# Performance work log

Hardware: AMD Instinct MI355X
Metric: run time of the kernel (lower is better)

Reference implementation:

```python
import jax, jax.numpy as jnp
import numpy as np

N = 100000
E = 1600000
H = 128
IN = 16
OUT = 16
L = 3
G = 256  # number of graphs
EPS = 1e-12


def setup_inputs() -> dict:
    key = jax.random.key(0)
    ks = jax.random.split(key, 24)
    s = 0.05
    inp = {
        "x": jax.random.normal(ks[0], (N, IN), jnp.float32),
        "pos": jax.random.normal(ks[1], (N, 3), jnp.float32),
        "edge_index": jax.random.randint(ks[2], (2, E), 0, N, jnp.int64),
        "batch": jnp.sort(jax.random.randint(ks[3], (N,), 0, G, jnp.int64)),
        # node_lin: Linear(IN,H), ReLU, Linear(H,H)
        "node_W1": jax.random.normal(ks[4], (IN, H), jnp.float32) * s,
        "node_b1": jnp.zeros((H,), jnp.float32),
        "node_W2": jax.random.normal(ks[5], (H, H), jnp.float32) * s,
        "node_b2": jnp.zeros((H,), jnp.float32),
        # per-layer local_nn: Linear(H+4,H), ReLU, Linear(H,H)  (stacked over L)
        "local_W1": jax.random.normal(ks[6], (L, H + 4, H), jnp.float32) * s,
        "local_b1": jnp.zeros((L, H), jnp.float32),
        "local_W2": jax.random.normal(ks[7], (L, H, H), jnp.float32) * s,
        "local_b2": jnp.zeros((L, H), jnp.float32),
        # per-layer global_nn: Linear(H,H), ReLU, Linear(H,H)
        "global_W1": jax.random.normal(ks[8], (L, H, H), jnp.float32) * s,
        "global_b1": jnp.zeros((L, H), jnp.float32),
        "global_W2": jax.random.normal(ks[9], (L, H, H), jnp.float32) * s,
        "global_b2": jnp.zeros((L, H), jnp.float32),
        # heads
        "lin1_W": jax.random.normal(ks[10], (H, H // 2), jnp.float32) * s,
        "lin1_b": jnp.zeros((H // 2,), jnp.float32),
        "lin2_W": jax.random.normal(ks[11], (H // 2, OUT), jnp.float32) * s,
        "lin2_b": jnp.zeros((OUT,), jnp.float32),
    }
    return inp


def _angle(v1, v2):
    c = jnp.cross(v1, v2, axis=1)
    return jnp.arctan2(jnp.linalg.norm(c, axis=1), jnp.sum(v1 * v2, axis=1))


def reference(x, pos, edge_index, batch,
              node_W1, node_b1, node_W2, node_b2,
              local_W1, local_b1, local_W2, local_b2,
              global_W1, global_b1, global_W2, global_b2,
              lin1_W, lin1_b, lin2_W, lin2_b):
    src = edge_index[0]  # j (source)
    dst = edge_index[1]  # i (target, aggregation index)

    normal = pos / (jnp.linalg.norm(pos, axis=-1, keepdims=True) + EPS)

    pos_i, pos_j = pos[dst], pos[src]
    n_i, n_j = normal[dst], normal[src]
    pseudo = pos_j - pos_i  # [E, 3]
    # point-pair features [E, 4] (constant across layers since pos is fixed)
    ppf = jnp.stack([
        jnp.linalg.norm(pseudo, axis=1),
        _angle(n_i, pseudo),
        _angle(n_j, pseudo),
        _angle(n_i, n_j),
    ], axis=1)

    # node_lin (x is 2D -> MLP path; embedding path unused)
    h = jax.nn.relu(x @ node_W1 + node_b1) @ node_W2 + node_b2  # [N, H]

    for l in range(L):
        msg = jnp.concatenate([h[src], ppf], axis=1)  # [E, H+4]
        msg = jax.nn.relu(msg @ local_W1[l] + local_b1[l]) @ local_W2[l] + local_b2[l]
        agg = jax.ops.segment_sum(msg, dst, num_segments=N)  # scatter-add to nodes
        h = jax.nn.relu(agg @ global_W1[l] + global_b1[l]) @ global_W2[l] + global_b2[l]
        h = jax.nn.relu(h)

    out = jax.nn.relu(h @ lin1_W + lin1_b) @ lin2_W + lin2_b  # [N, OUT]
    return jax.ops.segment_sum(out, batch, num_segments=G)  # [G, OUT]
```

## Files before the change

### kernel.cpp

```cpp
#include <hip/hip_runtime.h>

#define NN 100000
#define NE 1600000
#define HD 128
#define NL 3
#define NG 256
#define NB 196
#define BCAP 56

typedef __attribute__((ext_vector_type(8))) short short8;
typedef __attribute__((ext_vector_type(4))) float floatx4;
typedef __attribute__((ext_vector_type(2))) _Float16 half2v;

static __device__ __forceinline__ unsigned short f2bf(float f) {
    unsigned int u = __float_as_uint(f);
    u += 0x7fffu + ((u >> 16) & 1u);
    return (unsigned short)(u >> 16);
}
static __device__ __forceinline__ float bf2f(unsigned short h) {
    return __uint_as_float(((unsigned int)h) << 16);
}
static __device__ __forceinline__ float angle3(float ax, float ay, float az,
                                               float bx, float by, float bz) {
    float cx = ay*bz - az*by;
    float cy = az*bx - ax*bz;
    float cz = ax*by - ay*bx;
    float cn = sqrtf(cx*cx + cy*cy + cz*cz);
    float d  = ax*bx + ay*by + az*bz;
    return atan2f(cn, d);
}

union U32H2 { unsigned int u; half2v h; };
static __device__ __forceinline__ half2v u2h(unsigned int x) { U32H2 t; t.u = x; return t.h; }
static __device__ __forceinline__ unsigned int h2u(half2v x) { U32H2 t; t.h = x; return t.u; }


struct PrepSrcs { const float* p[14]; };

__global__ void k_prep(PrepSrcs s, unsigned short* __restrict__ dst) {
    int mat = blockIdx.y;
    int N = (mat == 13) ? 64 : 128;
    int e = blockIdx.x * 256 + threadIdx.x;
    if (e >= N * 128) return;
    int n = e >> 7, k = e & 127;
    dst[mat * 16384 + n * 128 + k] = f2bf(s.p[mat][k * N + n]);
}


__global__ void k_pn(const float* __restrict__ pos, float4* __restrict__ pn, int n) {
    int i = blockIdx.x * blockDim.x + threadIdx.x;
    if (i >= n) return;
    float x = pos[3*i], y = pos[3*i+1], z = pos[3*i+2];
    float inv = 1.0f / (sqrtf(x*x + y*y + z*z) + 1e-12f);
    pn[2*i]   = make_float4(x, y, z, 0.0f);
    pn[2*i+1] = make_float4(x*inv, y*inv, z*inv, 0.0f);
}


__global__ __launch_bounds__(256) void k_bcount(const int* __restrict__ ei,
                                                int* __restrict__ bcnt, int e) {
    __shared__ int cnt[NB];
    int tid = threadIdx.x;
    for (int i = tid; i < NB; i += 256) cnt[i] = 0;
    __syncthreads();
    int i0 = blockIdx.x * 4096 + tid * 16;
    if (i0 < e) {
#pragma unroll
        for (int q = 0; q < 4; q++) {
            int4 d4 = *(const int4*)(ei + NE + i0 + q * 4);
            atomicAdd(&cnt[d4.x >> 9], 1);
            atomicAdd(&cnt[d4.y >> 9], 1);
            atomicAdd(&cnt[d4.z >> 9], 1);
            atomicAdd(&cnt[d4.w >> 9], 1);
        }
    }
    __syncthreads();
    for (int i = tid; i < NB; i += 256)
        if (cnt[i]) atomicAdd(&bcnt[i], cnt[i]);
}

__global__ void k_bscan(const int* __restrict__ bcnt, int* __restrict__ bbase,
                        int* __restrict__ bcursor, int* __restrict__ starts) {
    if (threadIdx.x == 0 && blockIdx.x == 0) {
        int acc = 0;
        for (int b = 0; b < NB; b++) {
            bbase[b] = acc; bcursor[b] = acc;
            acc += bcnt[b];
        }
        bbase[NB] = acc;
        starts[NN] = NE;
    }
}

__global__ __launch_bounds__(256) void k_bscatter(const int* __restrict__ ei,
                                                  int* __restrict__ bcursor,
                                                  unsigned int* __restrict__ bids, int e) {
    __shared__ int lcnt[NB];
    __shared__ unsigned int lbuf[NB * BCAP];
    int tid = threadIdx.x;
    for (int i = tid; i < NB; i += 256) lcnt[i] = 0;
    __syncthreads();
    int i0 = blockIdx.x * 4096 + tid * 16;
    if (i0 < e) {
#pragma unroll
        for (int q = 0; q < 4; q++) {
            int4 s4 = *(const int4*)(ei + i0 + q * 4);
            int4 d4 = *(const int4*)(ei + NE + i0 + q * 4);
            int ds[4] = {d4.x, d4.y, d4.z, d4.w};
            int ss[4] = {s4.x, s4.y, s4.z, s4.w};
#pragma unroll
            for (int r = 0; r < 4; r++) {
                int d = ds[r];
                int b = d >> 9;
                unsigned int w = ((unsigned int)(d & 511) << 17) | (unsigned int)ss[r];
                int pos = atomicAdd(&lcnt[b], 1);
                if (pos < BCAP) lbuf[b * BCAP + pos] = w;
                else { int p = atomicAdd(&bcursor[b], 1); bids[p] = w; }
            }
        }
    }
    __syncthreads();
    if (tid < NB) {
        int c = lcnt[tid];
        if (c > BCAP) c = BCAP;
        if (c > 0) {
            int base = atomicAdd(&bcursor[tid], c);
            for (int k = 0; k < c; k++) bids[base + k] = lbuf[tid * BCAP + k];
        }
    }
}

__global__ __launch_bounds__(256) void k_bfinal(const unsigned int* __restrict__ bids,
                                                const int* __restrict__ bbase,
                                                int* __restrict__ ssrc,
                                                int* __restrict__ sdst,
                                                int* __restrict__ starts,
                                                int* __restrict__ deg) {
    __shared__ int s1[512];
    __shared__ int s2[256];
    int tid = threadIdx.x;
    int b = blockIdx.x;
    int node0 = b << 9;
    int base0 = bbase[b];
    int cnt = bbase[b + 1] - base0;
    s1[2 * tid] = 0; s1[2 * tid + 1] = 0;
    __syncthreads();
    for (int j = tid; j < cnt; j += 256)
        atomicAdd(&s1[bids[base0 + j] >> 17], 1);
    __syncthreads();
    int a0 = s1[2 * tid], a1 = s1[2 * tid + 1];
    s2[tid] = a0 + a1;
    __syncthreads();
    for (int off = 1; off < 256; off <<= 1) {
        int v = (tid >= off) ? s2[tid - off] : 0;
        __syncthreads();
        s2[tid] += v;
        __syncthreads();
    }
    int pairBase = (tid ? s2[tid - 1] : 0);
    int e0 = base0 + pairBase;
    int e1 = e0 + a0;
    int n0 = node0 + 2 * tid;
    if (n0 < NN)     { starts[n0] = e0;     deg[n0] = a0; }
    if (n0 + 1 < NN) { starts[n0 + 1] = e1; deg[n0 + 1] = a1; }
    s1[2 * tid] = e0; s1[2 * tid + 1] = e1;
    __syncthreads();
    for (int j = tid; j < cnt; j += 256) {
        unsigned int w = bids[base0 + j];
        int loc = w >> 17;
        int src = (int)(w & 0x1ffffu);
        int p = atomicAdd(&s1[loc], 1);
        ssrc[p] = src;
        sdst[p] = node0 + loc;
    }
}

__global__ void k_ppf_sorted(const int* __restrict__ ssrc, const int* __restrict__ sdst,
                             const float4* __restrict__ pn,
                             uint2* __restrict__ sppf, int e) {
    int j = blockIdx.x * blockDim.x + threadIdx.x;
    if (j >= e) return;
    int s = ssrc[j];
    int d = sdst[j];
    float4 ps_ = pn[2*s], ns_ = pn[2*s+1];
    float4 pd_ = pn[2*d], nd_ = pn[2*d+1];
    float px = ps_.x - pd_.x;
    float py = ps_.y - pd_.y;
    float pz = ps_.z - pd_.z;
    float f0 = sqrtf(px*px + py*py + pz*pz);
    float f1 = angle3(nd_.x, nd_.y, nd_.z, px, py, pz);
    float f2 = angle3(ns_.x, ns_.y, ns_.z, px, py, pz);
    float f3 = angle3(nd_.x, nd_.y, nd_.z, ns_.x, ns_.y, ns_.z);
    half2v h01 = { (_Float16)f0, (_Float16)f1 };
    half2v h23 = { (_Float16)f2, (_Float16)f3 };
    uint2 w;
    w.x = h2u(h01);
    w.y = h2u(h23);
    sppf[j] = w;
}


__global__ void k_node_lin1(const float* __restrict__ x, const float* __restrict__ W1,
                            const float* __restrict__ b1, unsigned short* __restrict__ u, int n) {
    __shared__ float sW[16 * HD];
    __shared__ float sb[HD];
    __shared__ float sx[16 * 16];
    int tid = threadIdx.x;
    for (int idx = tid; idx < 16 * HD; idx += 256) sW[idx] = W1[idx];
    if (tid < HD) sb[tid] = b1[tid];
    int r0 = blockIdx.x * 16;
    for (int idx = tid; idx < 16 * 16; idx += 256) {
        int r = r0 + (idx >> 4);
        sx[idx] = (r < n) ? x[r * 16 + (idx & 15)] : 0.0f;
    }
    __syncthreads();
    int col = tid & 127;
    int rsub = tid >> 7;
    float wcol[16];
#pragma unroll
    for (int k = 0; k < 16; k++) wcol[k] = sW[k * HD + col];
    float bb = sb[col];
    for (int rr = rsub; rr < 16; rr += 2) {
        int r = r0 + rr;
        if (r >= n) break;
        float acc = bb;
#pragma unroll
        for (int k = 0; k < 16; k++) acc = fmaf(sx[rr * 16 + k], wcol[k], acc);
        u[r * HD + col] = f2bf(fmaxf(acc, 0.0f));
    }
}


#define SKT 136

struct ChainArgs {
    const unsigned short* W[4];
    const float* bias[4];
    int epi[4];
};

template <int NS, int NCL>
__global__ __launch_bounds__(256, 4) void k_chain(
    const unsigned short* __restrict__ in, ChainArgs ca,
    const int* __restrict__ deg, unsigned short* __restrict__ out, int n) {
    __shared__ unsigned short LB[128 * SKT];
    __shared__ float sbias[NS][128];
    int tid = threadIdx.x;
    int wave = tid >> 6, lane = tid & 63, quad = lane >> 4, m = lane & 15;
    int rowBase = wave * 32;
    int gBase = blockIdx.x * 128;
    floatx4 z = {0.0f, 0.0f, 0.0f, 0.0f};
    short8 a[2][4];
#pragma unroll
    for (int rt = 0; rt < 2; rt++) {
        int r = gBase + rowBase + rt * 16 + m;
        int rc = r < n ? r : n - 1;
        const unsigned short* ap = in + (size_t)rc * 128 + quad * 8;
#pragma unroll
        for (int s = 0; s < 4; s++) a[rt][s] = *(const short8*)(ap + s * 32);
    }
    if (tid < 128) {
#pragma unroll
        for (int s = 0; s < NS; s++)
            if (ca.epi[s]) sbias[s][tid] = ca.bias[s][tid];
    }
    float dvd[2][4];
#pragma unroll
    for (int rt = 0; rt < 2; rt++)
#pragma unroll
        for (int r = 0; r < 4; r++) {
            int gr = gBase + rowBase + rt * 16 + quad * 4 + r;
            dvd[rt][r] = (float)deg[gr < n ? gr : n - 1];
        }

#pragma unroll
    for (int st = 0; st < NS; st++) {
        const int NC = (st == NS - 1) ? NCL : 128;
        if (st > 0) {
#pragma unroll
            for (int rt = 0; rt < 2; rt++) {
                const unsigned short* tp = &LB[(rowBase + rt * 16 + m) * SKT + quad * 8];
#pragma unroll
                for (int s = 0; s < 4; s++) a[rt][s] = *(const short8*)(tp + s * 32);
            }
            __syncthreads();
        }
        for (int idx = tid; idx < NC * 16; idx += 256) {
            int c = idx >> 4, k8 = idx & 15;
            *(short8*)&LB[c * SKT + k8 * 8] = ((const short8*)ca.W[st])[idx];
        }
        __syncthreads();

        floatx4 acc[2][8];
#pragma unroll
        for (int rt = 0; rt < 2; rt++)
#pragma unroll
            for (int ct = 0; ct < 8; ct++) acc[rt][ct] = z;
#pragma unroll
        for (int ct = 0; ct < NC / 16; ct++) {
            const unsigned short* bp = &LB[(ct * 16 + m) * SKT + quad * 8];
#pragma unroll
            for (int s = 0; s < 4; s++) {
                short8 b = *(const short8*)(bp + s * 32);
                acc[0][ct] = __builtin_amdgcn_mfma_f32_16x16x32_bf16(a[0][s], b, acc[0][ct], 0, 0, 0);
                acc[1][ct] = __builtin_amdgcn_mfma_f32_16x16x32_bf16(a[1][s], b, acc[1][ct], 0, 0, 0);
            }
        }
        __syncthreads();

        int epi = ca.epi[st];
#pragma unroll
        for (int ct = 0; ct < NC / 16; ct++) {
            int col = ct * 16 + m;
            float bv = epi ? sbias[st][col] : 0.0f;
#pragma unroll
            for (int rt = 0; rt < 2; rt++) {
#pragma unroll
                for (int r = 0; r < 4; r++) {
                    float v = acc[rt][ct][r];
                    if (epi == 1) v += bv;
                    else if (epi == 2) v += dvd[rt][r] * bv;
                    else if (epi == 3) v = fmaxf(v + bv, 0.0f);
                    unsigned short bw = f2bf(v);
                    int row = rowBase + rt * 16 + quad * 4 + r;
                    if (st == NS - 1) {
                        int gr = gBase + row;
                        if (gr < n) out[(size_t)gr * NCL + col] = bw;
                    } else {
                        LB[row * SKT + col] = bw;
                    }
                }
            }
        }
        if (st < NS - 1) __syncthreads();
    }
}


#if __has_builtin(__builtin_amdgcn_fdot2)
#define HAVE_FDOT2 1
#else
#define HAVE_FDOT2 0
#endif

static __device__ __forceinline__ void agg_edge(unsigned int u, uint2 q,
                                                half2v wA0, half2v wB0, half2v wA1, half2v wB1,
                                                float2 bb, float& a0, float& a1) {
    float tlo = __uint_as_float(u << 16);
    float thi = __uint_as_float(u & 0xffff0000u);
#if HAVE_FDOT2
    half2v p01 = u2h(q.x), p23 = u2h(q.y);
    float g0 = __builtin_amdgcn_fdot2(p01, wA0,
               __builtin_amdgcn_fdot2(p23, wB0, bb.x + tlo, false), false);
    float g1 = __builtin_amdgcn_fdot2(p01, wA1,
               __builtin_amdgcn_fdot2(p23, wB1, bb.y + thi, false), false);
#else
    half2v p01 = u2h(q.x), p23 = u2h(q.y);
    float px = (float)p01.x, py = (float)p01.y, pz = (float)p23.x, pw = (float)p23.y;
    float g0 = fmaf(px, (float)wA0.x, fmaf(py, (float)wA0.y,
               fmaf(pz, (float)wB0.x, fmaf(pw, (float)wB0.y, bb.x + tlo))));
    float g1 = fmaf(px, (float)wA1.x, fmaf(py, (float)wA1.y,
               fmaf(pz, (float)wB1.x, fmaf(pw, (float)wB1.y, bb.y + thi))));
#endif
    a0 += fmaxf(g0, 0.0f);
    a1 += fmaxf(g1, 0.0f);
}

__global__ __launch_bounds__(256, 8) void k_agg(
    const int* __restrict__ starts, const int* __restrict__ ssrc,
    const uint2* __restrict__ sppf, const unsigned int* __restrict__ t,
    const float* __restrict__ W1p, const float* __restrict__ b1,
    unsigned int* __restrict__ S, int n) {
    int node = (blockIdx.x * 256 + threadIdx.x) >> 6;
    if (node >= n) return;
    int lane = threadIdx.x & 63;
    int c2 = lane * 2;
    float2 w0 = *(const float2*)(W1p + c2);
    float2 w1 = *(const float2*)(W1p + 128 + c2);
    float2 w2 = *(const float2*)(W1p + 256 + c2);
    float2 w3 = *(const float2*)(W1p + 384 + c2);
    float2 bb = *(const float2*)(b1 + c2);
    half2v wA0 = { (_Float16)w0.x, (_Float16)w1.x };
    half2v wB0 = { (_Float16)w2.x, (_Float16)w3.x };
    half2v wA1 = { (_Float16)w0.y, (_Float16)w1.y };
    half2v wB1 = { (_Float16)w2.y, (_Float16)w3.y };
    int e0 = __builtin_amdgcn_readfirstlane(starts[node]);
    int e1 = __builtin_amdgcn_readfirstlane(starts[node + 1]);
    float a0 = 0.0f, a1 = 0.0f;
    int e = e0;
    for (; e + 8 <= e1; e += 8) {
        int s0 = ssrc[e],     s1 = ssrc[e + 1], s2 = ssrc[e + 2], s3 = ssrc[e + 3];
        int s4 = ssrc[e + 4], s5 = ssrc[e + 5], s6 = ssrc[e + 6], s7 = ssrc[e + 7];
        uint2 q0 = sppf[e],     q1 = sppf[e + 1], q2 = sppf[e + 2], q3 = sppf[e + 3];
        uint2 q4 = sppf[e + 4], q5 = sppf[e + 5], q6 = sppf[e + 6], q7 = sppf[e + 7];
        unsigned int u0 = t[((unsigned)s0 << 6) | lane];
        unsigned int u1 = t[((unsigned)s1 << 6) | lane];
        unsigned int u2 = t[((unsigned)s2 << 6) | lane];
        unsigned int u3 = t[((unsigned)s3 << 6) | lane];
        unsigned int u4 = t[((unsigned)s4 << 6) | lane];
        unsigned int u5 = t[((unsigned)s5 << 6) | lane];
        unsigned int u6 = t[((unsigned)s6 << 6) | lane];
        unsigned int u7 = t[((unsigned)s7 << 6) | lane];
        agg_edge(u0, q0, wA0, wB0, wA1, wB1, bb, a0, a1);
        agg_edge(u1, q1, wA0, wB0, wA1, wB1, bb, a0, a1);
        agg_edge(u2, q2, wA0, wB0, wA1, wB1, bb, a0, a1);
        agg_edge(u3, q3, wA0, wB0, wA1, wB1, bb, a0, a1);
        agg_edge(u4, q4, wA0, wB0, wA1, wB1, bb, a0, a1);
        agg_edge(u5, q5, wA0, wB0, wA1, wB1, bb, a0, a1);
        agg_edge(u6, q6, wA0, wB0, wA1, wB1, bb, a0, a1);
        agg_edge(u7, q7, wA0, wB0, wA1, wB1, bb, a0, a1);
    }
    for (; e + 4 <= e1; e += 4) {
        int s0 = ssrc[e], s1 = ssrc[e + 1], s2 = ssrc[e + 2], s3 = ssrc[e + 3];
        uint2 q0 = sppf[e], q1 = sppf[e + 1], q2 = sppf[e + 2], q3 = sppf[e + 3];
        unsigned int u0 = t[((unsigned)s0 << 6) | lane];
        unsigned int u1 = t[((unsigned)s1 << 6) | lane];
        unsigned int u2 = t[((unsigned)s2 << 6) | lane];
        unsigned int u3 = t[((unsigned)s3 << 6) | lane];
        agg_edge(u0, q0, wA0, wB0, wA1, wB1, bb, a0, a1);
        agg_edge(u1, q1, wA0, wB0, wA1, wB1, bb, a0, a1);
        agg_edge(u2, q2, wA0, wB0, wA1, wB1, bb, a0, a1);
        agg_edge(u3, q3, wA0, wB0, wA1, wB1, bb, a0, a1);
    }
    for (; e < e1; e++) {
        int s0 = ssrc[e];
        uint2 q0 = sppf[e];
        unsigned int u0 = t[((unsigned)s0 << 6) | lane];
        agg_edge(u0, q0, wA0, wB0, wA1, wB1, bb, a0, a1);
    }
    unsigned int r = ((unsigned int)f2bf(a1) << 16) | f2bf(a0);
    S[(size_t)node * 64 + lane] = r;
}


__global__ void k_head2(const unsigned short* __restrict__ v, const float* __restrict__ W,
                        const float* __restrict__ b, const int* __restrict__ batch,
                        float* __restrict__ outg, int n) {
    __shared__ float sW[64 * 16];
    __shared__ float sb[16];
    __shared__ float sacc[64][17];
    __shared__ int sbid[64];
    int tid = threadIdx.x;
    for (int idx = tid; idx < 64 * 16; idx += 256) sW[idx] = W[idx];
    if (tid < 16) sb[tid] = b[tid];
    int r0 = blockIdx.x * 64;
    if (tid < 64) {
        int r = r0 + tid;
        sbid[tid] = (r < n) ? batch[r] : -1;
    }
    __syncthreads();
    int rl = tid >> 4, c = tid & 15;
#pragma unroll
    for (int i = 0; i < 4; i++) {
        int row = rl + i * 16;
        int r = r0 + row;
        float acc = 0.0f;
        if (r < n) {
            const unsigned int* vr = (const unsigned int*)(v + (size_t)r * 64);
            acc = sb[c];
#pragma unroll
            for (int k2 = 0; k2 < 32; k2++) {
                unsigned int u = vr[k2];
                acc = fmaf(__uint_as_float(u << 16), sW[(2 * k2) * 16 + c], acc);
                acc = fmaf(__uint_as_float(u & 0xffff0000u), sW[(2 * k2 + 1) * 16 + c], acc);
            }
        }
        sacc[row][c] = acc;
    }
    __syncthreads();
    if (tid < 16) {
        int cc = tid;
        float run = 0.0f;
        int cur = sbid[0];
        for (int row = 0; row < 64; row++) {
            int bid = sbid[row];
            if (bid != cur) {
                if (cur >= 0) atomicAdd(&outg[cur * 16 + cc], run);
                run = 0.0f;
                cur = bid;
            }
            run += sacc[row][cc];
        }
        if (cur >= 0) atomicAdd(&outg[cur * 16 + cc], run);
    }
}


extern "C" void kernel_launch(void* const* d_in, const int* in_sizes, int n_in,
                              void* d_out, int out_size, void* d_ws, size_t ws_size,
                              hipStream_t stream) {
    (void)in_sizes; (void)n_in; (void)out_size; (void)ws_size;
    const float* x    = (const float*)d_in[0];
    const float* pos  = (const float*)d_in[1];
    const int*   ei   = (const int*)d_in[2];
    const int*   batch= (const int*)d_in[3];
    const float* nW1  = (const float*)d_in[4];
    const float* nb1  = (const float*)d_in[5];
    const float* nW2  = (const float*)d_in[6];
    const float* nb2  = (const float*)d_in[7];
    const float* lW1  = (const float*)d_in[8];
    const float* lb1  = (const float*)d_in[9];
    const float* lW2  = (const float*)d_in[10];
    const float* lb2  = (const float*)d_in[11];
    const float* gW1  = (const float*)d_in[12];
    const float* gb1  = (const float*)d_in[13];
    const float* gW2  = (const float*)d_in[14];
    const float* gb2  = (const float*)d_in[15];
    const float* l1W  = (const float*)d_in[16];
    const float* l1b  = (const float*)d_in[17];
    const float* l2W  = (const float*)d_in[18];
    const float* l2b  = (const float*)d_in[19];
    float* outg = (float*)d_out;

    char* ws = (char*)d_ws;
    size_t off = 0;
    auto alloc = [&](size_t bytes) -> void* {
        void* p = ws + off;
        off = (off + bytes + 255) & ~(size_t)255;
        return p;
    };
    unsigned short* P0 = (unsigned short*)alloc((size_t)NN * HD * 2);
    unsigned short* P1 = (unsigned short*)alloc((size_t)NN * HD * 2);
    uint2* sppf  = (uint2*)alloc((size_t)NE * 8);
    int* ssrc    = (int*)alloc((size_t)NE * 4);
    int* sdst    = (int*)alloc((size_t)NE * 4);
    float4* pn   = (float4*)alloc((size_t)NN * 32);
    int* deg     = (int*)alloc((size_t)NN * 4);
    int* starts  = (int*)alloc((size_t)(NN + 2) * 4);
    int* bcnt    = (int*)alloc((size_t)(NB + 2) * 4);
    int* bbase   = (int*)alloc((size_t)(NB + 2) * 4);
    int* bcursor = (int*)alloc((size_t)(NB + 2) * 4);
    unsigned short* pw = (unsigned short*)alloc((size_t)14 * 16384 * 2);
    unsigned int* bids = (unsigned int*)P0;

    PrepSrcs ps;
    ps.p[0] = nW2;
    for (int l = 0; l < 3; l++) {
        ps.p[1 + l] = lW1 + (size_t)l * 132 * 128;
        ps.p[4 + l] = lW2 + (size_t)l * 16384;
        ps.p[7 + l] = gW1 + (size_t)l * 16384;
        ps.p[10 + l] = gW2 + (size_t)l * 16384;
    }
    ps.p[13] = l1W;

    hipMemsetAsync(bcnt, 0, (size_t)(NB + 2) * 4, stream);
    hipMemsetAsync(outg, 0, (size_t)NG * 16 * 4, stream);

    k_prep<<<dim3(64, 14), 256, 0, stream>>>(ps, pw);
    k_pn<<<(NN + 255) / 256, 256, 0, stream>>>(pos, pn, NN);
    const int NTILE = (NE + 4095) / 4096;
    k_bcount<<<NTILE, 256, 0, stream>>>(ei, bcnt, NE);
    k_bscan<<<1, 64, 0, stream>>>(bcnt, bbase, bcursor, starts);
    k_bscatter<<<NTILE, 256, 0, stream>>>(ei, bcursor, bids, NE);
    k_bfinal<<<NB, 256, 0, stream>>>(bids, bbase, ssrc, sdst, starts, deg);
    k_ppf_sorted<<<(NE + 255) / 256, 256, 0, stream>>>(ssrc, sdst, pn, sppf, NE);

    k_node_lin1<<<(NN + 15) / 16, 256, 0, stream>>>(x, nW1, nb1, P1, NN);

    const int GB = (NN + 127) / 128;
    const int AGB = (NN * 64 + 255) / 256;

    {
        ChainArgs ca;
        ca.W[0] = pw;                      ca.bias[0] = nb2;     ca.epi[0] = 1;
        ca.W[1] = pw + (size_t)1 * 16384;  ca.bias[1] = nullptr; ca.epi[1] = 0;
        ca.W[2] = nullptr; ca.bias[2] = nullptr; ca.epi[2] = 0;
        ca.W[3] = nullptr; ca.bias[3] = nullptr; ca.epi[3] = 0;
        k_chain<2, 128><<<GB, 256, 0, stream>>>(P1, ca, deg, P0, NN);
    }

    unsigned short* tbuf = P0;
    unsigned short* sbuf = P1;
    for (int l = 0; l < NL; l++) {
        const float* W1p = lW1 + (size_t)l * 132 * 128 + 128 * 128;
        const float* b1  = lb1 + l * 128;
        k_agg<<<AGB, 256, 0, stream>>>(starts, ssrc, sppf, (const unsigned int*)tbuf,
                                       W1p, b1, (unsigned int*)sbuf, NN);
        ChainArgs ca;
        ca.W[0] = pw + (size_t)(4 + l) * 16384;  ca.bias[0] = lb2 + l * 128; ca.epi[0] = 2;
        ca.W[1] = pw + (size_t)(7 + l) * 16384;  ca.bias[1] = gb1 + l * 128; ca.epi[1] = 3;
        ca.W[2] = pw + (size_t)(10 + l) * 16384; ca.bias[2] = gb2 + l * 128; ca.epi[2] = 3;
        if (l < NL - 1) {
            ca.W[3] = pw + (size_t)(2 + l) * 16384;
            ca.bias[3] = nullptr; ca.epi[3] = 0;
            k_chain<4, 128><<<GB, 256, 0, stream>>>(sbuf, ca, deg, tbuf, NN);
        } else {
            ca.W[3] = pw + (size_t)13 * 16384;
            ca.bias[3] = l1b; ca.epi[3] = 3;
            k_chain<4, 64><<<GB, 256, 0, stream>>>(sbuf, ca, deg, tbuf, NN);
        }
    }
    k_head2<<<(NN + 63) / 64, 256, 0, stream>>>(tbuf, l2W, l2b, batch, outg, NN);
}
```

Before: 523.7 us.

## Replace count+scan bucketing with fixed-capacity buckets and fold local bias into chain

Removes the count and scan kernels for the edge bucket sort by giving each bucket a fixed-capacity region, so the scatter runs directly after a tiny cursor init. Edge arrays become padded, so the ppf kernel skips unused slots, and k_agg uses starts plus degree instead of starts[node+1]. The local_nn first-layer bias is moved into the preceding chain GEMM epilogue, removing a per-edge add in aggregation. The trade-off is that the fixed per-bucket capacity assumes a bounded in-degree per bucket, padded arrays get larger, and sdst now reuses the P1 buffer.

```diff
diff --git a/kernel.cpp b/kernel.cpp
--- a/kernel.cpp
+++ b/kernel.cpp
@@ -7,6 +7,7 @@
 #define NG 256
 #define NB 196
 #define BCAP 56
+#define BCAPTOT 10240
 
 typedef __attribute__((ext_vector_type(8))) short short8;
 typedef __attribute__((ext_vector_type(4))) float floatx4;
@@ -57,39 +58,9 @@
 }
 
 
-__global__ __launch_bounds__(256) void k_bcount(const int* __restrict__ ei,
-                                                int* __restrict__ bcnt, int e) {
-    __shared__ int cnt[NB];
-    int tid = threadIdx.x;
-    for (int i = tid; i < NB; i += 256) cnt[i] = 0;
-    __syncthreads();
-    int i0 = blockIdx.x * 4096 + tid * 16;
-    if (i0 < e) {
-#pragma unroll
-        for (int q = 0; q < 4; q++) {
-            int4 d4 = *(const int4*)(ei + NE + i0 + q * 4);
-            atomicAdd(&cnt[d4.x >> 9], 1);
-            atomicAdd(&cnt[d4.y >> 9], 1);
-            atomicAdd(&cnt[d4.z >> 9], 1);
-            atomicAdd(&cnt[d4.w >> 9], 1);
-        }
-    }
-    __syncthreads();
-    for (int i = tid; i < NB; i += 256)
-        if (cnt[i]) atomicAdd(&bcnt[i], cnt[i]);
-}
-
-__global__ void k_bscan(const int* __restrict__ bcnt, int* __restrict__ bbase,
-                        int* __restrict__ bcursor, int* __restrict__ starts) {
-    if (threadIdx.x == 0 && blockIdx.x == 0) {
-        int acc = 0;
-        for (int b = 0; b < NB; b++) {
-            bbase[b] = acc; bcursor[b] = acc;
-            acc += bcnt[b];
-        }
-        bbase[NB] = acc;
-        starts[NN] = NE;
-    }
+__global__ void k_binit(int* __restrict__ bcursor) {
+    int b = threadIdx.x;
+    if (b < NB) bcursor[b] = b * BCAPTOT;
 }
 
 __global__ __launch_bounds__(256) void k_bscatter(const int* __restrict__ ei,
@@ -131,7 +102,7 @@
 }
 
 __global__ __launch_bounds__(256) void k_bfinal(const unsigned int* __restrict__ bids,
-                                                const int* __restrict__ bbase,
+                                                const int* __restrict__ bcursor,
                                                 int* __restrict__ ssrc,
                                                 int* __restrict__ sdst,
                                                 int* __restrict__ starts,
@@ -141,8 +112,8 @@
     int tid = threadIdx.x;
     int b = blockIdx.x;
     int node0 = b << 9;
-    int base0 = bbase[b];
-    int cnt = bbase[b + 1] - base0;
+    int base0 = b * BCAPTOT;
+    int cnt = bcursor[b] - base0;
     s1[2 * tid] = 0; s1[2 * tid + 1] = 0;
     __syncthreads();
     for (int j = tid; j < cnt; j += 256)
@@ -177,11 +148,12 @@
 
 __global__ void k_ppf_sorted(const int* __restrict__ ssrc, const int* __restrict__ sdst,
                              const float4* __restrict__ pn,
-                             uint2* __restrict__ sppf, int e) {
+                             uint2* __restrict__ sppf, int npos) {
     int j = blockIdx.x * blockDim.x + threadIdx.x;
-    if (j >= e) return;
-    int s = ssrc[j];
-    int d = sdst[j];
+    if (j >= npos) return;
+    unsigned int s = (unsigned int)ssrc[j];
+    unsigned int d = (unsigned int)sdst[j];
+    if (s >= NN || d >= NN) return;
     float4 ps_ = pn[2*s], ns_ = pn[2*s+1];
     float4 pd_ = pn[2*d], nd_ = pn[2*d+1];
     float px = ps_.x - pd_.x;
@@ -345,31 +317,32 @@
 
 static __device__ __forceinline__ void agg_edge(unsigned int u, uint2 q,
                                                 half2v wA0, half2v wB0, half2v wA1, half2v wB1,
-                                                float2 bb, float& a0, float& a1) {
+                                                float& a0, float& a1) {
     float tlo = __uint_as_float(u << 16);
     float thi = __uint_as_float(u & 0xffff0000u);
 #if HAVE_FDOT2
     half2v p01 = u2h(q.x), p23 = u2h(q.y);
     float g0 = __builtin_amdgcn_fdot2(p01, wA0,
-               __builtin_amdgcn_fdot2(p23, wB0, bb.x + tlo, false), false);
+               __builtin_amdgcn_fdot2(p23, wB0, tlo, false), false);
     float g1 = __builtin_amdgcn_fdot2(p01, wA1,
-               __builtin_amdgcn_fdot2(p23, wB1, bb.y + thi, false), false);
+               __builtin_amdgcn_fdot2(p23, wB1, thi, false), false);
 #else
     half2v p01 = u2h(q.x), p23 = u2h(q.y);
     float px = (float)p01.x, py = (float)p01.y, pz = (float)p23.x, pw = (float)p23.y;
     float g0 = fmaf(px, (float)wA0.x, fmaf(py, (float)wA0.y,
-               fmaf(pz, (float)wB0.x, fmaf(pw, (float)wB0.y, bb.x + tlo))));
+               fmaf(pz, (float)wB0.x, fmaf(pw, (float)wB0.y, tlo))));
     float g1 = fmaf(px, (float)wA1.x, fmaf(py, (float)wA1.y,
-               fmaf(pz, (float)wB1.x, fmaf(pw, (float)wB1.y, bb.y + thi))));
+               fmaf(pz, (float)wB1.x, fmaf(pw, (float)wB1.y, thi))));
 #endif
     a0 += fmaxf(g0, 0.0f);
     a1 += fmaxf(g1, 0.0f);
 }
 
 __global__ __launch_bounds__(256, 8) void k_agg(
-    const int* __restrict__ starts, const int* __restrict__ ssrc,
+    const int* __restrict__ starts, const int* __restrict__ deg,
+    const int* __restrict__ ssrc,
     const uint2* __restrict__ sppf, const unsigned int* __restrict__ t,
-    const float* __restrict__ W1p, const float* __restrict__ b1,
+    const float* __restrict__ W1p,
     unsigned int* __restrict__ S, int n) {
     int node = (blockIdx.x * 256 + threadIdx.x) >> 6;
     if (node >= n) return;
@@ -379,13 +352,13 @@
     float2 w1 = *(const float2*)(W1p + 128 + c2);
     float2 w2 = *(const float2*)(W1p + 256 + c2);
     float2 w3 = *(const float2*)(W1p + 384 + c2);
-    float2 bb = *(const float2*)(b1 + c2);
     half2v wA0 = { (_Float16)w0.x, (_Float16)w1.x };
     half2v wB0 = { (_Float16)w2.x, (_Float16)w3.x };
     half2v wA1 = { (_Float16)w0.y, (_Float16)w1.y };
     half2v wB1 = { (_Float16)w2.y, (_Float16)w3.y };
     int e0 = __builtin_amdgcn_readfirstlane(starts[node]);
-    int e1 = __builtin_amdgcn_readfirstlane(starts[node + 1]);
+    int dg = __builtin_amdgcn_readfirstlane(deg[node]);
+    int e1 = e0 + dg;
     float a0 = 0.0f, a1 = 0.0f;
     int e = e0;
     for (; e + 8 <= e1; e += 8) {
@@ -401,14 +374,15 @@
         unsigned int u5 = t[((unsigned)s5 << 6) | lane];
         unsigned int u6 = t[((unsigned)s6 << 6) | lane];
         unsigned int u7 = t[((unsigned)s7 << 6) | lane];
-        agg_edge(u0, q0, wA0, wB0, wA1, wB1, bb, a0, a1);
-        agg_edge(u1, q1, wA0, wB0, wA1, wB1, bb, a0, a1);
-        agg_edge(u2, q2, wA0, wB0, wA1, wB1, bb, a0, a1);
-        agg_edge(u3, q3, wA0, wB0, wA1, wB1, bb, a0, a1);
-        agg_edge(u4, q4, wA0, wB0, wA1, wB1, bb, a0, a1);
-        agg_edge(u5, q5, wA0, wB0, wA1, wB1, bb, a0, a1);
-        agg_edge(u6, q6, wA0, wB0, wA1, wB1, bb, a0, a1);
-        agg_edge(u7, q7, wA0, wB0, wA1, wB1, bb, a0, a1);
+        __asm__ __volatile__("" ::: "memory");
+        agg_edge(u0, q0, wA0, wB0, wA1, wB1, a0, a1);
+        agg_edge(u1, q1, wA0, wB0, wA1, wB1, a0, a1);
+        agg_edge(u2, q2, wA0, wB0, wA1, wB1, a0, a1);
+        agg_edge(u3, q3, wA0, wB0, wA1, wB1, a0, a1);
+        agg_edge(u4, q4, wA0, wB0, wA1, wB1, a0, a1);
+        agg_edge(u5, q5, wA0, wB0, wA1, wB1, a0, a1);
+        agg_edge(u6, q6, wA0, wB0, wA1, wB1, a0, a1);
+        agg_edge(u7, q7, wA0, wB0, wA1, wB1, a0, a1);
     }
     for (; e + 4 <= e1; e += 4) {
         int s0 = ssrc[e], s1 = ssrc[e + 1], s2 = ssrc[e + 2], s3 = ssrc[e + 3];
@@ -417,16 +391,17 @@
         unsigned int u1 = t[((unsigned)s1 << 6) | lane];
         unsigned int u2 = t[((unsigned)s2 << 6) | lane];
         unsigned int u3 = t[((unsigned)s3 << 6) | lane];
-        agg_edge(u0, q0, wA0, wB0, wA1, wB1, bb, a0, a1);
-        agg_edge(u1, q1, wA0, wB0, wA1, wB1, bb, a0, a1);
-        agg_edge(u2, q2, wA0, wB0, wA1, wB1, bb, a0, a1);
-        agg_edge(u3, q3, wA0, wB0, wA1, wB1, bb, a0, a1);
+        __asm__ __volatile__("" ::: "memory");
+        agg_edge(u0, q0, wA0, wB0, wA1, wB1, a0, a1);
+        agg_edge(u1, q1, wA0, wB0, wA1, wB1, a0, a1);
+        agg_edge(u2, q2, wA0, wB0, wA1, wB1, a0, a1);
+        agg_edge(u3, q3, wA0, wB0, wA1, wB1, a0, a1);
     }
     for (; e < e1; e++) {
         int s0 = ssrc[e];
         uint2 q0 = sppf[e];
         unsigned int u0 = t[((unsigned)s0 << 6) | lane];
-        agg_edge(u0, q0, wA0, wB0, wA1, wB1, bb, a0, a1);
+        agg_edge(u0, q0, wA0, wB0, wA1, wB1, a0, a1);
     }
     unsigned int r = ((unsigned int)f2bf(a1) << 16) | f2bf(a0);
     S[(size_t)node * 64 + lane] = r;
@@ -512,6 +487,8 @@
     const float* l2b  = (const float*)d_in[19];
     float* outg = (float*)d_out;
 
+    const int NPOS = NB * BCAPTOT;
+
     char* ws = (char*)d_ws;
     size_t off = 0;
     auto alloc = [&](size_t bytes) -> void* {
@@ -521,17 +498,15 @@
     };
     unsigned short* P0 = (unsigned short*)alloc((size_t)NN * HD * 2);
     unsigned short* P1 = (unsigned short*)alloc((size_t)NN * HD * 2);
-    uint2* sppf  = (uint2*)alloc((size_t)NE * 8);
-    int* ssrc    = (int*)alloc((size_t)NE * 4);
-    int* sdst    = (int*)alloc((size_t)NE * 4);
+    uint2* sppf  = (uint2*)alloc((size_t)NPOS * 8);
+    int* ssrc    = (int*)alloc((size_t)NPOS * 4);
     float4* pn   = (float4*)alloc((size_t)NN * 32);
     int* deg     = (int*)alloc((size_t)NN * 4);
     int* starts  = (int*)alloc((size_t)(NN + 2) * 4);
-    int* bcnt    = (int*)alloc((size_t)(NB + 2) * 4);
-    int* bbase   = (int*)alloc((size_t)(NB + 2) * 4);
     int* bcursor = (int*)alloc((size_t)(NB + 2) * 4);
     unsigned short* pw = (unsigned short*)alloc((size_t)14 * 16384 * 2);
     unsigned int* bids = (unsigned int*)P0;
+    int* sdst          = (int*)P1;
 
     PrepSrcs ps;
     ps.p[0] = nW2;
@@ -543,17 +518,15 @@
     }
     ps.p[13] = l1W;
 
-    hipMemsetAsync(bcnt, 0, (size_t)(NB + 2) * 4, stream);
     hipMemsetAsync(outg, 0, (size_t)NG * 16 * 4, stream);
 
     k_prep<<<dim3(64, 14), 256, 0, stream>>>(ps, pw);
     k_pn<<<(NN + 255) / 256, 256, 0, stream>>>(pos, pn, NN);
+    k_binit<<<1, 256, 0, stream>>>(bcursor);
     const int NTILE = (NE + 4095) / 4096;
-    k_bcount<<<NTILE, 256, 0, stream>>>(ei, bcnt, NE);
-    k_bscan<<<1, 64, 0, stream>>>(bcnt, bbase, bcursor, starts);
     k_bscatter<<<NTILE, 256, 0, stream>>>(ei, bcursor, bids, NE);
-    k_bfinal<<<NB, 256, 0, stream>>>(bids, bbase, ssrc, sdst, starts, deg);
-    k_ppf_sorted<<<(NE + 255) / 256, 256, 0, stream>>>(ssrc, sdst, pn, sppf, NE);
+    k_bfinal<<<NB, 256, 0, stream>>>(bids, bcursor, ssrc, sdst, starts, deg);
+    k_ppf_sorted<<<(NPOS + 255) / 256, 256, 0, stream>>>(ssrc, sdst, pn, sppf, NPOS);
 
     k_node_lin1<<<(NN + 15) / 16, 256, 0, stream>>>(x, nW1, nb1, P1, NN);
 
@@ -562,8 +535,8 @@
 
     {
         ChainArgs ca;
-        ca.W[0] = pw;                      ca.bias[0] = nb2;     ca.epi[0] = 1;
-        ca.W[1] = pw + (size_t)1 * 16384;  ca.bias[1] = nullptr; ca.epi[1] = 0;
+        ca.W[0] = pw;                      ca.bias[0] = nb2;  ca.epi[0] = 1;
+        ca.W[1] = pw + (size_t)1 * 16384;  ca.bias[1] = lb1;  ca.epi[1] = 1;
         ca.W[2] = nullptr; ca.bias[2] = nullptr; ca.epi[2] = 0;
         ca.W[3] = nullptr; ca.bias[3] = nullptr; ca.epi[3] = 0;
         k_chain<2, 128><<<GB, 256, 0, stream>>>(P1, ca, deg, P0, NN);
@@ -573,16 +546,17 @@
     unsigned short* sbuf = P1;
     for (int l = 0; l < NL; l++) {
         const float* W1p = lW1 + (size_t)l * 132 * 128 + 128 * 128;
-        const float* b1  = lb1 + l * 128;
-        k_agg<<<AGB, 256, 0, stream>>>(starts, ssrc, sppf, (const unsigned int*)tbuf,
-                                       W1p, b1, (unsigned int*)sbuf, NN);
+        k_agg<<<AGB, 256, 0, stream>>>(starts, deg, ssrc, sppf,
+                                       (const unsigned int*)tbuf, W1p,
+                                       (unsigned int*)sbuf, NN);
         ChainArgs ca;
         ca.W[0] = pw + (size_t)(4 + l) * 16384;  ca.bias[0] = lb2 + l * 128; ca.epi[0] = 2;
         ca.W[1] = pw + (size_t)(7 + l) * 16384;  ca.bias[1] = gb1 + l * 128; ca.epi[1] = 3;
         ca.W[2] = pw + (size_t)(10 + l) * 16384; ca.bias[2] = gb2 + l * 128; ca.epi[2] = 3;
         if (l < NL - 1) {
             ca.W[3] = pw + (size_t)(2 + l) * 16384;
-            ca.bias[3] = nullptr; ca.epi[3] = 0;
+            ca.bias[3] = lb1 + (l + 1) * 128;
+            ca.epi[3] = 1;
             k_chain<4, 128><<<GB, 256, 0, stream>>>(sbuf, ca, deg, tbuf, NN);
         } else {
             ca.W[3] = pw + (size_t)13 * 16384;
```

Result: faster. 507.7 us, median of 2 (-3.1%).
